# Optimization experiments

Hardware: AMD Instinct MI355X
Metric: run time of the kernel (lower is better)

## Reference

```python
import jax, jax.numpy as jnp
import numpy as np

DEPTH = 8  # remaining_depth at the root
N_INTERNAL = 2**DEPTH - 1  # 255, level-order indexed
N_LEAF = 2**DEPTH          # 256
CLAMP_MIN = 1e-5


def setup_inputs() -> dict:
    key = jax.random.key(0)
    k1, k2, k3 = jax.random.split(key, 3)
    B, D_in, D_out = 65536, 1024, 128
    x = jax.random.normal(k1, (B, D_in), dtype=jnp.float32)
    # one independent Linear(D_in,1) per internal node (deepcopy of split_function),
    # packed into a single [D_in, N_INTERNAL] matrix, level-order
    W_split = jax.random.normal(k2, (D_in, N_INTERNAL), dtype=jnp.float32) * (1.0 / np.sqrt(D_in))
    b_split = jnp.zeros((N_INTERNAL,), dtype=jnp.float32)
    # leaf values: uniform(-a, a) with a = sqrt(6/output_dim), per the torch init
    a = (6.0 / D_out) ** 0.5
    leaf_values = jax.random.uniform(k3, (N_LEAF, D_out), minval=-a, maxval=a, dtype=jnp.float32)
    return {"x": x, "W_split": W_split, "b_split": b_split, "leaf_values": leaf_values}


def reference(x, W_split, b_split, leaf_values):
    B = x.shape[0]
    # gate probability of every internal node in one batched GEMM: [B, N_INTERNAL]
    P = jax.nn.sigmoid(x @ W_split + b_split)
    # accumulate soft routing probability to each leaf, level by level
    probs = jnp.ones((B, 1), dtype=x.dtype)
    for d in range(DEPTH):
        p = P[:, 2**d - 1 : 2**(d + 1) - 1]  # gates at level d: [B, 2^d]
        # child order: left = (1-p), right = p (matches recursion ordering)
        probs = jnp.stack([(1.0 - p) * probs, p * probs], axis=-1).reshape(B, 2**(d + 1))
    out = probs @ leaf_values  # [B, D_out]: sum_leaf path_prob * value
    # regularization: sum over internal nodes of -0.5 * 2^-depth * mean_b log(clamp(p(1-p)))
    weights = jnp.concatenate(
        [jnp.full((2**d,), 2.0 ** (-d), dtype=x.dtype) for d in range(DEPTH)]
    )  # [N_INTERNAL]
    reg = jnp.sum(-0.5 * weights * jnp.mean(jnp.log(jnp.maximum(P * (1.0 - P), CLAMP_MIN)), axis=0))
    return out, reg
```

## Files before the change

kernel.cpp:

```cpp
#include <hip/hip_runtime.h>

#define B_TOT   65536
#define DIN     1024
#define NNODES  255
#define NPAD    256
#define DOUT    128
#define BM      128
#define BK      64
#define NKT     (DIN / BK)

typedef __attribute__((ext_vector_type(8))) _Float16      f16x8;
typedef __attribute__((ext_vector_type(4))) float         f32x4;
typedef __attribute__((ext_vector_type(4))) unsigned short u16x4;
typedef __attribute__((ext_vector_type(8))) unsigned short u16x8;
typedef unsigned short u16;
typedef unsigned int   u32;

__device__ __forceinline__ u16 f2h(float f) {
  _Float16 h = (_Float16)f;
  return __builtin_bit_cast(u16, h);
}
__device__ __forceinline__ float h2f(u16 b) {
  return (float)__builtin_bit_cast(_Float16, b);
}
__device__ __forceinline__ u32 pk2h(float a, float b) {
  return __builtin_bit_cast(u32, __builtin_amdgcn_cvt_pkrtz(a, b));
}

__device__ __forceinline__ int swz64(int row, int col) {
  return (row << 6) + ((((col >> 3) ^ row) & 7) << 3) + (col & 7);
}
__device__ __forceinline__ int swzP(int row, int col) {
  int g = col >> 3;
  int gs = (g & ~7) | ((g ^ row) & 7);
  return (row << 8) + (gs << 3) + (col & 7);
}

__global__ void prep_w(const float* __restrict__ Wsp, u16* __restrict__ WtG) {
  __shared__ float t[64][65];
  const int tid = threadIdx.x;
  const int wn = blockIdx.x;
  const int kc = blockIdx.y;
  const int bn = wn * 64, bk = kc * 64;
  {
    int n = tid & 63, kr0 = tid >> 6;
    #pragma unroll
    for (int i = 0; i < 16; ++i) {
      int k = kr0 + i * 4;
      int node = bn + n;
      t[k][n] = (node < NNODES) ? Wsp[(size_t)(bk + k) * NNODES + node] : 0.0f;
    }
  }
  __syncthreads();
  #pragma unroll
  for (int half = 0; half < 2; ++half) {
    int f = half * 256 + tid;
    int nt = f >> 7, rem = f & 127;
    int ks = rem >> 6, rem2 = rem & 63;
    int quad = rem2 >> 4, l15 = rem2 & 15;
    int nl = nt * 16 + l15;
    u16x8 v;
    #pragma unroll
    for (int j = 0; j < 8; ++j)
      v[j] = f2h(t[ks * 32 + quad * 8 + j][nl]);
    size_t F = (size_t)((((kc * 4 + wn) * 4 + nt) * 2 + ks) * 64 + (quad * 16 + l15));
    *(u16x8*)&WtG[F * 8] = v;
  }
}

__global__ void prep_leaf(const float* __restrict__ leaf, u16* __restrict__ lT) {
  int t = blockIdx.x * 256 + threadIdx.x;
  int j = t & 127, l = t >> 7;
  lT[j * NPAD + l] = f2h(leaf[l * DOUT + j]);
}

__global__ __launch_bounds__(512, 4) void fused_sdt(
    const float* __restrict__ x, const float* __restrict__ bsp,
    const u16* __restrict__ WtG, const u16* __restrict__ lT,
    float* __restrict__ out, float* __restrict__ regp)
{
  __shared__ char smem[65536] __attribute__((aligned(16)));
  u16* xs0 = (u16*)smem;
  u16* xs1 = xs0 + 8192;
  u16* PB  = (u16*)smem;

  const int tid  = threadIdx.x;
  const int lane = tid & 63;
  const int w    = tid >> 6;
  const int l15  = lane & 15;
  const int quad = lane >> 4;
  const int wm   = w >> 2;
  const int wn   = w & 3;
  const int blk  = blockIdx.x;

  const float* xg = x + (size_t)blk * BM * DIN;

  f32x4 acc[4][4];
  #pragma unroll
  for (int mt = 0; mt < 4; ++mt)
    #pragma unroll
    for (int nt = 0; nt < 4; ++nt) {
      f32x4 z = {0.0f, 0.0f, 0.0f, 0.0f};
      acc[mt][nt] = z;
    }

  {
    #pragma unroll
    for (int i = 0; i < 4; ++i) {
      int idx = i * 512 + tid;
      int row = idx >> 4, kg = idx & 15;
      float4 v = *(const float4*)(xg + (size_t)row * DIN + kg * 4);
      u32 lo = pk2h(v.x, v.y);
      u32 hi = pk2h(v.z, v.w);
      u16x4 h;
      h.x = lo & 0xffff; h.y = lo >> 16;
      h.z = hi & 0xffff; h.w = hi >> 16;
      *(u16x4*)&xs0[swz64(row, kg * 4)] = h;
    }
  }
  __syncthreads();

  u16* xcur = xs0;
  u16* xnxt = xs1;
  for (int kc = 0; kc < NKT; ++kc) {
    float4 xv[4];
    const bool pf = (kc + 1 < NKT);
    if (pf) {
      #pragma unroll
      for (int i = 0; i < 4; ++i) {
        int idx = i * 512 + tid;
        int row = idx >> 4, kg = idx & 15;
        xv[i] = *(const float4*)(xg + (size_t)row * DIN + (kc + 1) * BK + kg * 4);
      }
    }
    const u16* wbase = WtG + (size_t)kc * 16384 + (size_t)wn * 4096;
    __builtin_amdgcn_s_setprio(1);
    #pragma unroll
    for (int ks = 0; ks < 2; ++ks) {
      const int kk = ks * 32 + quad * 8;
      f16x8 A[4], Bf[4];
      #pragma unroll
      for (int nt = 0; nt < 4; ++nt)
        Bf[nt] = *(const f16x8*)&wbase[nt * 1024 + ks * 512 + lane * 8];
      #pragma unroll
      for (int mt = 0; mt < 4; ++mt)
        A[mt] = *(const f16x8*)&xcur[swz64(wm * 64 + mt * 16 + l15, kk)];
      #pragma unroll
      for (int mt = 0; mt < 4; ++mt)
        #pragma unroll
        for (int nt = 0; nt < 4; ++nt)
          acc[mt][nt] = __builtin_amdgcn_mfma_f32_16x16x32_f16(
              A[mt], Bf[nt], acc[mt][nt], 0, 0, 0);
    }
    __builtin_amdgcn_s_setprio(0);
    if (pf) {
      #pragma unroll
      for (int i = 0; i < 4; ++i) {
        int idx = i * 512 + tid;
        int row = idx >> 4, kg = idx & 15;
        u32 lo = pk2h(xv[i].x, xv[i].y);
        u32 hi = pk2h(xv[i].z, xv[i].w);
        u16x4 h;
        h.x = lo & 0xffff; h.y = lo >> 16;
        h.z = hi & 0xffff; h.w = hi >> 16;
        *(u16x4*)&xnxt[swz64(row, kg * 4)] = h;
      }
    }
    __syncthreads();
    u16* tsw = xcur; xcur = xnxt; xnxt = tsw;
  }

  float rsum = 0.0f;
  float bv[4];
  #pragma unroll
  for (int nt = 0; nt < 4; ++nt) {
    int c = wn * 64 + nt * 16 + l15;
    bv[nt] = (c < NNODES) ? bsp[c] : 0.0f;
  }
  #pragma unroll
  for (int mt = 0; mt < 4; ++mt) {
    #pragma unroll
    for (int nt = 0; nt < 4; ++nt) {
      int c = wn * 64 + nt * 16 + l15;
      #pragma unroll
      for (int r = 0; r < 4; ++r) {
        int row = wm * 64 + mt * 16 + quad * 4 + r;
        float z = acc[mt][nt][r] + bv[nt];
        float e = __expf(-z);
        float p = __builtin_amdgcn_rcpf(1.0f + e);
        PB[swzP(row, c)] = f2h(p);
        if (c < NNODES) {
          float v = fmaxf(p * (1.0f - p), 1e-5f);
          int d = 31 - __clz(c + 1);
          float wgt = __builtin_bit_cast(float, (u32)(127 - d) << 23);
          rsum += wgt * __logf(v);
        }
      }
    }
  }
  #pragma unroll
  for (int off = 32; off > 0; off >>= 1) rsum += __shfl_down(rsum, off, 64);
  if (lane == 0) atomicAdd(regp, rsum * (-0.5f / 65536.0f));
  __syncthreads();

  for (int rr = 0; rr < 16; ++rr) {
    int row = (w << 4) + rr;
    float prod = 1.0f;
    #pragma unroll
    for (int d = 0; d < 6; ++d) {
      int node = (1 << d) - 1 + (lane >> (6 - d));
      float pv = h2f(PB[swzP(row, node)]);
      prod *= ((lane >> (5 - d)) & 1) ? pv : (1.0f - pv);
    }
    float p6  = h2f(PB[swzP(row, 63 + lane)]);
    float p7a = h2f(PB[swzP(row, 127 + 2 * lane)]);
    float p7b = h2f(PB[swzP(row, 128 + 2 * lane)]);
    float a0 = prod * (1.0f - p6), a1 = prod * p6;
    u16x4 o;
    o.x = f2h(a0 * (1.0f - p7a));
    o.y = f2h(a0 * p7a);
    o.z = f2h(a1 * (1.0f - p7b));
    o.w = f2h(a1 * p7b);
    *(u16x4*)&PB[swzP(row, 4 * lane)] = o;
  }
  __syncthreads();

  f32x4 acc2[4][2];
  #pragma unroll
  for (int mt = 0; mt < 4; ++mt)
    #pragma unroll
    for (int nt = 0; nt < 2; ++nt) {
      f32x4 z = {0.0f, 0.0f, 0.0f, 0.0f};
      acc2[mt][nt] = z;
    }
  for (int kc = 0; kc < 4; ++kc) {
    #pragma unroll
    for (int ks = 0; ks < 2; ++ks) {
      const int kk = kc * 64 + ks * 32 + quad * 8;
      f16x8 Af[4], Bf2[2];
      #pragma unroll
      for (int nt = 0; nt < 2; ++nt)
        Bf2[nt] = *(const f16x8*)&lT[(wn * 32 + nt * 16 + l15) * NPAD + kk];
      #pragma unroll
      for (int mt = 0; mt < 4; ++mt)
        Af[mt] = *(const f16x8*)&PB[swzP(wm * 64 + mt * 16 + l15, kk)];
      #pragma unroll
      for (int mt = 0; mt < 4; ++mt)
        #pragma unroll
        for (int nt = 0; nt < 2; ++nt)
          acc2[mt][nt] = __builtin_amdgcn_mfma_f32_16x16x32_f16(
              Af[mt], Bf2[nt], acc2[mt][nt], 0, 0, 0);
    }
  }
  #pragma unroll
  for (int mt = 0; mt < 4; ++mt)
    #pragma unroll
    for (int nt = 0; nt < 2; ++nt)
      #pragma unroll
      for (int r = 0; r < 4; ++r) {
        int row = wm * 64 + mt * 16 + quad * 4 + r;
        int col = wn * 32 + nt * 16 + l15;
        out[(size_t)(blk * BM + row) * DOUT + col] = acc2[mt][nt][r];
      }
}

extern "C" void kernel_launch(void* const* d_in, const int* in_sizes, int n_in,
                              void* d_out, int out_size, void* d_ws, size_t ws_size,
                              hipStream_t stream) {
  (void)in_sizes; (void)n_in; (void)out_size; (void)ws_size;
  const float* x    = (const float*)d_in[0];
  const float* Wsp  = (const float*)d_in[1];
  const float* bsp  = (const float*)d_in[2];
  const float* leaf = (const float*)d_in[3];
  float* out  = (float*)d_out;
  float* regp = out + (size_t)B_TOT * DOUT;

  u16* WtG = (u16*)d_ws;
  u16* lT  = WtG + NPAD * DIN;

  (void)hipMemsetAsync(regp, 0, sizeof(float), stream);
  prep_w<<<dim3(4, 16), 256, 0, stream>>>(Wsp, WtG);
  prep_leaf<<<(NPAD * DOUT) / 256, 256, 0, stream>>>(leaf, lT);
  fused_sdt<<<B_TOT / BM, 512, 0, stream>>>(x, bsp, WtG, lT, out, regp);
}
```

Before: 473.2 us.

## Register double-buffer W fragments across k-tiles and replace reg atomics with partials

Measured after the change: 687.1 us. +45.2%, slower.

```diff
diff --git a/kernel.cpp b/kernel.cpp
--- a/kernel.cpp
+++ b/kernel.cpp
@@ -74,10 +74,28 @@
   lT[j * NPAD + l] = f2h(leaf[l * DOUT + j]);
 }
 
+__global__ void finalize(const float* __restrict__ pw, float* __restrict__ regp) {
+  int t = threadIdx.x;
+  float s = 0.0f;
+  #pragma unroll
+  for (int i = 0; i < 8; ++i) s += pw[i * 512 + t];
+  #pragma unroll
+  for (int off = 32; off > 0; off >>= 1) s += __shfl_down(s, off, 64);
+  __shared__ float red[8];
+  if ((t & 63) == 0) red[t >> 6] = s;
+  __syncthreads();
+  if (t == 0) {
+    float tot = 0.0f;
+    #pragma unroll
+    for (int i = 0; i < 8; ++i) tot += red[i];
+    *regp = tot * (-0.5f / 65536.0f);
+  }
+}
+
 __global__ __launch_bounds__(512, 4) void fused_sdt(
     const float* __restrict__ x, const float* __restrict__ bsp,
     const u16* __restrict__ WtG, const u16* __restrict__ lT,
-    float* __restrict__ out, float* __restrict__ regp)
+    float* __restrict__ out, float* __restrict__ pw)
 {
   __shared__ char smem[65536] __attribute__((aligned(16)));
   u16* xs0 = (u16*)smem;
@@ -103,6 +121,14 @@
       f32x4 z = {0.0f, 0.0f, 0.0f, 0.0f};
       acc[mt][nt] = z;
     }
+
+  f16x8 BfA[8], BfB[8];
+  {
+    const u16* wb = WtG + (size_t)wn * 4096;
+    #pragma unroll
+    for (int q = 0; q < 8; ++q)
+      BfA[q] = *(const f16x8*)&wb[(q & 3) * 1024 + (q >> 2) * 512 + lane * 8];
+  }
 
   {
     #pragma unroll
@@ -122,9 +148,15 @@
 
   u16* xcur = xs0;
   u16* xnxt = xs1;
-  for (int kc = 0; kc < NKT; ++kc) {
+  auto ktile = [&](f16x8 (&Bc)[8], f16x8 (&Bn)[8], int kc) {
+    const bool pf = (kc + 1 < NKT);
+    if (pf) {
+      const u16* wb = WtG + (size_t)(kc + 1) * 16384 + (size_t)wn * 4096;
+      #pragma unroll
+      for (int q = 0; q < 8; ++q)
+        Bn[q] = *(const f16x8*)&wb[(q & 3) * 1024 + (q >> 2) * 512 + lane * 8];
+    }
     float4 xv[4];
-    const bool pf = (kc + 1 < NKT);
     if (pf) {
       #pragma unroll
       for (int i = 0; i < 4; ++i) {
@@ -133,15 +165,11 @@
         xv[i] = *(const float4*)(xg + (size_t)row * DIN + (kc + 1) * BK + kg * 4);
       }
     }
-    const u16* wbase = WtG + (size_t)kc * 16384 + (size_t)wn * 4096;
     __builtin_amdgcn_s_setprio(1);
     #pragma unroll
     for (int ks = 0; ks < 2; ++ks) {
       const int kk = ks * 32 + quad * 8;
-      f16x8 A[4], Bf[4];
-      #pragma unroll
-      for (int nt = 0; nt < 4; ++nt)
-        Bf[nt] = *(const f16x8*)&wbase[nt * 1024 + ks * 512 + lane * 8];
+      f16x8 A[4];
       #pragma unroll
       for (int mt = 0; mt < 4; ++mt)
         A[mt] = *(const f16x8*)&xcur[swz64(wm * 64 + mt * 16 + l15, kk)];
@@ -150,7 +178,7 @@
         #pragma unroll
         for (int nt = 0; nt < 4; ++nt)
           acc[mt][nt] = __builtin_amdgcn_mfma_f32_16x16x32_f16(
-              A[mt], Bf[nt], acc[mt][nt], 0, 0, 0);
+              A[mt], Bc[ks * 4 + nt], acc[mt][nt], 0, 0, 0);
     }
     __builtin_amdgcn_s_setprio(0);
     if (pf) {
@@ -168,6 +196,10 @@
     }
     __syncthreads();
     u16* tsw = xcur; xcur = xnxt; xnxt = tsw;
+  };
+  for (int kc = 0; kc < NKT; kc += 2) {
+    ktile(BfA, BfB, kc);
+    ktile(BfB, BfA, kc + 1);
   }
 
   float rsum = 0.0f;
@@ -200,7 +232,7 @@
   }
   #pragma unroll
   for (int off = 32; off > 0; off >>= 1) rsum += __shfl_down(rsum, off, 64);
-  if (lane == 0) atomicAdd(regp, rsum * (-0.5f / 65536.0f));
+  if (lane == 0) pw[blk * 8 + w] = rsum;
   __syncthreads();
 
   for (int rr = 0; rr < 16; ++rr) {
@@ -277,9 +309,10 @@
 
   u16* WtG = (u16*)d_ws;
   u16* lT  = WtG + NPAD * DIN;
-
-  (void)hipMemsetAsync(regp, 0, sizeof(float), stream);
+  float* pw = (float*)(lT + NPAD * DOUT);
+
   prep_w<<<dim3(4, 16), 256, 0, stream>>>(Wsp, WtG);
   prep_leaf<<<(NPAD * DOUT) / 256, 256, 0, stream>>>(leaf, lT);
-  fused_sdt<<<B_TOT / BM, 512, 0, stream>>>(x, bsp, WtG, lT, out, regp);
-}
+  fused_sdt<<<B_TOT / BM, 512, 0, stream>>>(x, bsp, WtG, lT, out, pw);
+  finalize<<<1, 512, 0, stream>>>(pw, regp);
+}
```
